# Performance work log

Hardware: AMD Instinct MI355X
Metric: run time of the kernel (lower is better)

## Reference

```python
import jax, jax.numpy as jnp
import numpy as np

TEXT_DIM = 768
IMAGE_DIM = 1024
HIDDEN = 2048
FF = 128
HEADS = 8
HEAD_DIM = HIDDEN // HEADS  # 256


def setup_inputs() -> dict:
    key = jax.random.key(0)
    ks = jax.random.split(key, 16)
    def lin(k, fan_in, fan_out):
        bound = 1.0 / np.sqrt(fan_in)
        kw, kb = jax.random.split(k)
        W = jax.random.uniform(kw, (fan_in, fan_out), jnp.float32, -bound, bound)
        b = jax.random.uniform(kb, (fan_out,), jnp.float32, -bound, bound)
        return W, b
    text = jax.random.normal(ks[0], (16, 512, TEXT_DIM), jnp.float32)
    image = jax.random.normal(ks[1], (16, 576, IMAGE_DIM), jnp.float32)
    wq, bq = lin(ks[2], TEXT_DIM, HIDDEN)
    wk, bk = lin(ks[3], IMAGE_DIM, HIDDEN)
    wv, bv = lin(ks[4], IMAGE_DIM, HIDDEN)
    wr, br = lin(ks[5], HIDDEN, TEXT_DIM)
    w1, b1 = lin(ks[6], TEXT_DIM, FF)
    w2, b2 = lin(ks[7], FF, TEXT_DIM)
    gamma = jnp.ones((TEXT_DIM,), jnp.float32)
    beta = jnp.zeros((TEXT_DIM,), jnp.float32)
    return {"text": text, "image": image,
            "wq": wq, "bq": bq, "wk": wk, "bk": bk, "wv": wv, "bv": bv,
            "wr": wr, "br": br, "w1": w1, "b1": b1, "w2": w2, "b2": b2,
            "gamma": gamma, "beta": beta}


def reference(text, image, wq, bq, wk, bk, wv, bv, wr, br, w1, b1, w2, b2, gamma, beta):
    # Dropout is identity (eval mode).
    bs, lt, _ = text.shape
    li = image.shape[1]
    Q = (text @ wq + bq).reshape(bs, lt, HEADS, HEAD_DIM)
    K = (image @ wk + bk).reshape(bs, li, HEADS, HEAD_DIM)
    V = (image @ wv + bv).reshape(bs, li, HEADS, HEAD_DIM)
    scale = jnp.sqrt(jnp.float32(HEAD_DIM))
    scores = jnp.einsum('bqhd,bkhd->bhqk', Q, K) / scale  # [B,H,Lt,Li]
    attn = jax.nn.softmax(scores, axis=-1)
    x = jnp.einsum('bhqk,bkhd->bqhd', attn, V).reshape(bs, lt, HIDDEN)
    out = x @ wr + br  # [B,Lt,text_dim]
    ff = jax.nn.relu(out @ w1 + b1) @ w2 + b2
    out = out + ff
    # LayerNorm over last dim (eps=1e-5, torch default)
    mu = jnp.mean(out, axis=-1, keepdims=True)
    var = jnp.mean(jnp.square(out - mu), axis=-1, keepdims=True)
    return (out - mu) / jnp.sqrt(var + 1e-5) * gamma + beta
```

## Files before the change

### kernel.cpp

```cpp
#include <hip/hip_runtime.h>
#include <stdint.h>
#include <stddef.h>

typedef __attribute__((ext_vector_type(8))) short bf16x8;
typedef __attribute__((ext_vector_type(4))) float f32x4;

typedef __attribute__((address_space(1))) unsigned int uint_g;
typedef __attribute__((address_space(3))) unsigned int uint_l;

#define DEV static __device__ __forceinline__

DEV unsigned short f2bf(float f) {
  unsigned int u = __float_as_uint(f);
  u += 0x7FFFu + ((u >> 16) & 1u);
  return (unsigned short)(u >> 16);
}

DEV void gl_lds16(const unsigned short* g, unsigned short* l) {
  __builtin_amdgcn_global_load_lds((const uint_g*)g, (uint_l*)l, 16, 0, 0);
}

__global__ __launch_bounds__(256) void k_f32_to_bf16(const float* __restrict__ in,
                                                     unsigned short* __restrict__ out, int n4) {
  int i = blockIdx.x * 256 + threadIdx.x;
  if (i >= n4) return;
  const float4 v = ((const float4*)in)[i];
  ushort4 o;
  o.x = f2bf(v.x); o.y = f2bf(v.y); o.z = f2bf(v.z); o.w = f2bf(v.w);
  ((ushort4*)out)[i] = o;
}

__global__ __launch_bounds__(256) void k_transpose_to_bf16(const float* __restrict__ in,
                                                           unsigned short* __restrict__ out,
                                                           int R, int C) {
  __shared__ unsigned short tile[32][33];
  const int c0 = blockIdx.x << 5, r0 = blockIdx.y << 5;
  const int tx = threadIdx.x & 31, ty = threadIdx.x >> 5;
  #pragma unroll
  for (int i = 0; i < 32; i += 8)
    tile[ty + i][tx] = f2bf(in[(size_t)(r0 + ty + i) * C + c0 + tx]);
  __syncthreads();
  #pragma unroll
  for (int i = 0; i < 32; i += 8)
    out[(size_t)(c0 + ty + i) * R + r0 + tx] = tile[tx][ty + i];
}

enum { EPI_BIAS = 0, EPI_VT = 3, EPI_DUAL = 4, EPI_RELU = 5, EPI_RES = 6, EPI_KV = 7 };

template <int EPI>
DEV void gemm8_body(unsigned short (&As)[2][16384], unsigned short (&Bs)[2][16384],
                    const unsigned short* __restrict__ A, const unsigned short* __restrict__ B,
                    int lda, int ldb, int kTiles,
                    void* C0, void* C1, const float* bias, const float* bias2,
                    int ldc, float scale, int bx, int by) {
  const int t = threadIdx.x;
  const int lane = t & 63, w = t >> 6;
  const int wm = w >> 2, wn = w & 3;
  const int frow = lane & 15, quad = lane >> 4;

  const unsigned short* Ab = A + (size_t)by * 256 * lda;
  const unsigned short* Bb = B + (size_t)bx * 256 * ldb;

  f32x4 acc[8][4] = {};

  auto stA = [&](int kt, int bi, int h) {
    #pragma unroll
    for (int it = 0; it < 2; ++it) {
      int e = (it << 9) + t;
      int row = (h << 7) + (e >> 3);
      int c16 = (e & 7) ^ (row & 7);
      gl_lds16(Ab + (size_t)row * lda + (kt << 6) + (c16 << 3),
               &As[bi][(row << 6) + ((e & 7) << 3)]);
    }
  };
  auto stB = [&](int kt, int bi, int h) {
    #pragma unroll
    for (int it = 0; it < 2; ++it) {
      int e = (it << 9) + t;
      int row = (h << 7) + (e >> 3);
      int c16 = (e & 7) ^ (row & 7);
      gl_lds16(Bb + (size_t)row * ldb + (kt << 6) + (c16 << 3),
               &Bs[bi][(row << 6) + ((e & 7) << 3)]);
    }
  };
  auto frag = [&](const unsigned short* buf, int row, int ksl) -> bf16x8 {
    int col = ((ksl << 5) + (quad << 3)) ^ ((row & 7) << 3);
    return *(const bf16x8*)&buf[(row << 6) + col];
  };

  stB(0, 0, 0); stB(0, 0, 1); stA(0, 0, 0); stA(0, 0, 1);
  if (kTiles > 1) {
    stB(1, 1, 0); stB(1, 1, 1); stA(1, 1, 0);
    asm volatile("s_waitcnt vmcnt(6)" ::: "memory");
  } else {
    asm volatile("s_waitcnt vmcnt(0)" ::: "memory");
  }
  asm volatile("s_barrier" ::: "memory");

  bf16x8 a[4][2], b0[2][2], b1[2][2];
  const int arow = wm << 7, brow = wn << 6;

  for (int kt = 0; kt < kTiles; ++kt) {
    const int pb = kt & 1, qb = pb ^ 1;
    const unsigned short* Ac = As[pb];
    const unsigned short* Bc = Bs[pb];

    #pragma unroll
    for (int m = 0; m < 4; ++m)
      #pragma unroll
      for (int k = 0; k < 2; ++k) a[m][k] = frag(Ac, arow + (m << 4) + frow, k);
    #pragma unroll
    for (int n = 0; n < 2; ++n)
      #pragma unroll
      for (int k = 0; k < 2; ++k) b0[n][k] = frag(Bc, brow + (n << 4) + frow, k);
    if (kt + 1 < kTiles) stA(kt + 1, qb, 1);
    asm volatile("s_barrier" ::: "memory");
    asm volatile("s_waitcnt lgkmcnt(0)" ::: "memory");
    __builtin_amdgcn_s_setprio(1);
    #pragma unroll
    for (int m = 0; m < 4; ++m)
      #pragma unroll
      for (int n = 0; n < 2; ++n)
        #pragma unroll
        for (int k = 0; k < 2; ++k)
          acc[m][n] = __builtin_amdgcn_mfma_f32_16x16x32_bf16(a[m][k], b0[n][k], acc[m][n], 0, 0, 0);
    __builtin_amdgcn_s_setprio(0);
    asm volatile("s_barrier" ::: "memory");

    #pragma unroll
    for (int n = 0; n < 2; ++n)
      #pragma unroll
      for (int k = 0; k < 2; ++k) b1[n][k] = frag(Bc, brow + 32 + (n << 4) + frow, k);
    if (kt + 2 < kTiles) stB(kt + 2, pb, 0);
    asm volatile("s_barrier" ::: "memory");
    asm volatile("s_waitcnt lgkmcnt(0)" ::: "memory");
    __builtin_amdgcn_s_setprio(1);
    #pragma unroll
    for (int m = 0; m < 4; ++m)
      #pragma unroll
      for (int n = 0; n < 2; ++n)
        #pragma unroll
        for (int k = 0; k < 2; ++k)
          acc[m][2 + n] = __builtin_amdgcn_mfma_f32_16x16x32_bf16(a[m][k], b1[n][k], acc[m][2 + n], 0, 0, 0);
    __builtin_amdgcn_s_setprio(0);
    asm volatile("s_barrier" ::: "memory");

    #pragma unroll
    for (int m = 0; m < 4; ++m)
      #pragma unroll
      for (int k = 0; k < 2; ++k) a[m][k] = frag(Ac, arow + 64 + (m << 4) + frow, k);
    if (kt + 2 < kTiles) stB(kt + 2, pb, 1);
    asm volatile("s_barrier" ::: "memory");
    asm volatile("s_waitcnt lgkmcnt(0)" ::: "memory");
    __builtin_amdgcn_s_setprio(1);
    #pragma unroll
    for (int m = 0; m < 4; ++m)
      #pragma unroll
      for (int n = 0; n < 2; ++n)
        #pragma unroll
        for (int k = 0; k < 2; ++k)
          acc[4 + m][n] = __builtin_amdgcn_mfma_f32_16x16x32_bf16(a[m][k], b0[n][k], acc[4 + m][n], 0, 0, 0);
    __builtin_amdgcn_s_setprio(0);
    asm volatile("s_barrier" ::: "memory");

    if (kt + 2 < kTiles) {
      stA(kt + 2, pb, 0);
      asm volatile("s_waitcnt vmcnt(6)" ::: "memory");
    } else if (kt + 1 < kTiles) {
      asm volatile("s_waitcnt vmcnt(0)" ::: "memory");
    }
    asm volatile("s_barrier" ::: "memory");
    __builtin_amdgcn_s_setprio(1);
    #pragma unroll
    for (int m = 0; m < 4; ++m)
      #pragma unroll
      for (int n = 0; n < 2; ++n)
        #pragma unroll
        for (int k = 0; k < 2; ++k)
          acc[4 + m][2 + n] = __builtin_amdgcn_mfma_f32_16x16x32_bf16(a[m][k], b1[n][k], acc[4 + m][2 + n], 0, 0, 0);
    __builtin_amdgcn_s_setprio(0);
    asm volatile("s_barrier" ::: "memory");
  }

  const int mb = by * 256 + wm * 128 + (quad << 2);
  const int nb = bx * 256 + wn * 64 + frow;
  #pragma unroll
  for (int mi = 0; mi < 8; ++mi) {
    const int m = mb + mi * 16;
    #pragma unroll
    for (int ni = 0; ni < 4; ++ni) {
      const int n = nb + ni * 16;
      f32x4 v = acc[mi][ni];
      if constexpr (EPI == EPI_BIAS) {
        unsigned short* O = (unsigned short*)C0;
        const float bv2 = bias[n];
        #pragma unroll
        for (int r = 0; r < 4; ++r) O[(size_t)(m + r) * ldc + n] = f2bf((v[r] + bv2) * scale);
      } else if constexpr (EPI == EPI_KV) {
        if (n < 2048) {
          unsigned short* O = (unsigned short*)C0;
          const float bv2 = bias[n];
          #pragma unroll
          for (int r = 0; r < 4; ++r) O[(size_t)(m + r) * ldc + n] = f2bf(v[r] + bv2);
        } else {
          const int n2 = n - 2048;
          const int b = m / 576, li = m - b * 576;
          const int h = n2 >> 8, d = n2 & 255;
          const float bv2 = bias2[n2];
          ushort4 o;
          o.x = f2bf(v[0] + bv2); o.y = f2bf(v[1] + bv2);
          o.z = f2bf(v[2] + bv2); o.w = f2bf(v[3] + bv2);
          *(ushort4*)((unsigned short*)C1 + ((size_t)((b * 8 + h) * 256 + d)) * 576 + li) = o;
        }
      }
    }
  }
}

__global__ __launch_bounds__(512, 2)
void k_qkv(const unsigned short* __restrict__ Tbf, const unsigned short* __restrict__ wqT,
           unsigned short* Qb, const float* bq, float qscale,
           const unsigned short* __restrict__ Ibf, const unsigned short* __restrict__ wkT,
           unsigned short* Kb, unsigned short* Vt, const float* bk, const float* bv) {
  __shared__ unsigned short As[2][16384];
  __shared__ unsigned short Bs[2][16384];
  const int id = blockIdx.x;
  if (id < 576) {
    gemm8_body<EPI_KV>(As, Bs, Ibf, wkT, 1024, 1024, 16,
                       Kb, Vt, bk, bv, 2048, 1.0f, id & 15, id >> 4);
  } else {
    const int q = id - 576;
    gemm8_body<EPI_BIAS>(As, Bs, Tbf, wqT, 768, 768, 12,
                         Qb, nullptr, bq, nullptr, 2048, qscale, q & 7, q >> 3);
  }
}

template <int BM, int BN, int EPI>
__global__ __launch_bounds__(256)
void k_gemm(const unsigned short* __restrict__ A, const unsigned short* __restrict__ B,
            int lda, int ldb, int kSteps,
            void* C0, void* C1, const float* bias, const float* resid, int ldc, float scale) {
  constexpr int TM = BM / 32;
  constexpr int TN = BN / 32;
  __shared__ unsigned short At[2][BM * 32];
  __shared__ unsigned short Bt[2][BN * 32];

  const int t = threadIdx.x;
  const int lane = t & 63, wave = t >> 6;
  const int wm = wave >> 1, wn = wave & 1;

  const unsigned short* Ab = A + (size_t)blockIdx.y * BM * lda;
  const unsigned short* Bb = B + (size_t)blockIdx.x * BN * ldb;

  const int frow = lane & 15, fk = (lane >> 4) << 3;

  f32x4 acc[TM][TN] = {};

  auto stage = [&](int ks, int bi) {
    const int k0 = ks << 5;
    #pragma unroll
    for (int r = 0; r < BM / 64; ++r) {
      int off16 = (r << 8) + t;
      int row = off16 >> 2, kk = (off16 & 3) << 3;
      gl_lds16(Ab + (size_t)row * lda + k0 + kk, &At[bi][(row << 5) + kk]);
    }
    #pragma unroll
    for (int r = 0; r < BN / 64; ++r) {
      int off16 = (r << 8) + t;
      int row = off16 >> 2, kk = (off16 & 3) << 3;
      gl_lds16(Bb + (size_t)row * ldb + k0 + kk, &Bt[bi][(row << 5) + kk]);
    }
  };

  stage(0, 0);

  for (int ks = 0; ks < kSteps; ++ks) {
    const int buf = ks & 1;
    __syncthreads();
    if (ks + 1 < kSteps) stage(ks + 1, buf ^ 1);

    bf16x8 af[TM], bv[TN];
    #pragma unroll
    for (int mi = 0; mi < TM; ++mi)
      af[mi] = *(const bf16x8*)&At[buf][((wm * (BM / 2) + mi * 16 + frow) << 5) + fk];
    #pragma unroll
    for (int ni = 0; ni < TN; ++ni)
      bv[ni] = *(const bf16x8*)&Bt[buf][((wn * (BN / 2) + ni * 16 + frow) << 5) + fk];
    #pragma unroll
    for (int mi = 0; mi < TM; ++mi)
      #pragma unroll
      for (int ni = 0; ni < TN; ++ni)
        acc[mi][ni] = __builtin_amdgcn_mfma_f32_16x16x32_bf16(af[mi], bv[ni], acc[mi][ni], 0, 0, 0);
  }

  const int mb = blockIdx.y * BM + wm * (BM / 2) + ((lane >> 4) << 2);
  const int nb = blockIdx.x * BN + wn * (BN / 2) + (lane & 15);

  #pragma unroll
  for (int mi = 0; mi < TM; ++mi) {
    const int m = mb + mi * 16;
    #pragma unroll
    for (int ni = 0; ni < TN; ++ni) {
      const int n = nb + ni * 16;
      f32x4 v = acc[mi][ni];
      if constexpr (EPI == EPI_BIAS) {
        unsigned short* O = (unsigned short*)C0;
        const float bv2 = bias[n];
        #pragma unroll
        for (int r = 0; r < 4; ++r) O[(size_t)(m + r) * ldc + n] = f2bf((v[r] + bv2) * scale);
      } else if constexpr (EPI == EPI_DUAL) {
        float* Of = (float*)C0;
        unsigned short* Ob = (unsigned short*)C1;
        const float bv2 = bias[n];
        #pragma unroll
        for (int r = 0; r < 4; ++r) {
          const float x = v[r] + bv2;
          const size_t idx = (size_t)(m + r) * ldc + n;
          Of[idx] = x; Ob[idx] = f2bf(x);
        }
      } else if constexpr (EPI == EPI_RELU) {
        unsigned short* O = (unsigned short*)C0;
        const float bv2 = bias[n];
        #pragma unroll
        for (int r = 0; r < 4; ++r) {
          const float x = v[r] + bv2;
          O[(size_t)(m + r) * ldc + n] = f2bf(x > 0.f ? x : 0.f);
        }
      } else if constexpr (EPI == EPI_RES) {
        float* Of = (float*)C0;
        const float bv2 = bias[n];
        #pragma unroll
        for (int r = 0; r < 4; ++r) {
          const size_t idx = (size_t)(m + r) * ldc + n;
          Of[idx] = v[r] + bv2 + resid[idx];
        }
      }
    }
  }
}

__global__ __launch_bounds__(512, 2)
void k_flash(const unsigned short* __restrict__ Q, const unsigned short* __restrict__ K,
             const unsigned short* __restrict__ Vt, unsigned short* __restrict__ X) {
  __shared__ unsigned short Ks[2][8 * 32 * 32];
  __shared__ unsigned short Vs[2][256 * 32];
  __shared__ unsigned short Ps[256 * 40];
  __shared__ unsigned short Ones[512];

  const int t = threadIdx.x, lane = t & 63, w = t >> 6;
  const int frow = lane & 15, quad = lane >> 4, fk = quad << 3;

  const int id = blockIdx.x;
  const int qb = (id >> 3) & 1;
  const int bh = (id & 7) | ((id >> 4) << 3);
  const int b = bh >> 3, h = bh & 7;
  const int q0 = qb << 8;

  const unsigned short* Kg = K + ((size_t)b * 576) * 2048 + h * 256;
  const unsigned short* Vg = Vt + (size_t)bh * 147456;

  Ones[t] = (t < 32) ? (unsigned short)0x3F80 : (unsigned short)0;

  bf16x8 Qf[2][8];
  #pragma unroll
  for (int half = 0; half < 2; ++half) {
    const unsigned short* Qg =
        Q + ((size_t)(b * 512 + q0 + w * 32 + half * 16 + frow)) * 2048 + h * 256;
    #pragma unroll
    for (int kd = 0; kd < 8; ++kd)
      Qf[half][kd] = *(const bf16x8*)(Qg + kd * 32 + fk);
  }

  f32x4 acc_o[2][17] = {};

  auto stage = [&](int s, int bi) {
    const int li0 = s << 5;
    unsigned short* Kb = &Ks[bi][0];
    unsigned short* Vb = &Vs[bi][0];
    #pragma unroll
    for (int it = 0; it < 2; ++it) {
      int e = (it << 9) + t;
      int row = e >> 2, c = (e & 3) << 3;
      int kd = row >> 5, li = row & 31;
      gl_lds16(Kg + (size_t)(li0 + li) * 2048 + kd * 32 + c, &Kb[(row << 5) + c]);
    }
    #pragma unroll
    for (int it = 0; it < 2; ++it) {
      int e = (it << 9) + t;
      int d = e >> 2, c = (e & 3) << 3;
      gl_lds16(Vg + (size_t)d * 576 + li0 + c, &Vb[(d << 5) + c]);
    }
  };

  stage(0, 0);

  const int prow = (w << 5) + (quad << 2);

  for (int s = 0; s < 18; ++s) {
    const int buf = s & 1;
    __syncthreads();
    if (s + 1 < 18) stage(s + 1, buf ^ 1);

    f32x4 acc_s[2][2] = {};
    #pragma unroll
    for (int kd = 0; kd < 8; ++kd) {
      #pragma unroll
      for (int ni = 0; ni < 2; ++ni) {
        const bf16x8 bv = *(const bf16x8*)&Ks[buf][((kd * 32 + ni * 16 + frow) << 5) + fk];
        acc_s[0][ni] = __builtin_amdgcn_mfma_f32_16x16x32_bf16(Qf[0][kd], bv, acc_s[0][ni], 0, 0, 0);
        acc_s[1][ni] = __builtin_amdgcn_mfma_f32_16x16x32_bf16(Qf[1][kd], bv, acc_s[1][ni], 0, 0, 0);
      }
    }

    #pragma unroll
    for (int half = 0; half < 2; ++half)
      #pragma unroll
      for (int ni = 0; ni < 2; ++ni)
        #pragma unroll
        for (int r = 0; r < 4; ++r)
          Ps[(prow + half * 16 + r) * 40 + ni * 16 + frow] =
              f2bf(__builtin_amdgcn_exp2f(acc_s[half][ni][r]));

    bf16x8 paf[2];
    paf[0] = *(const bf16x8*)&Ps[((w << 5) + frow) * 40 + fk];
    paf[1] = *(const bf16x8*)&Ps[((w << 5) + 16 + frow) * 40 + fk];
    #pragma unroll
    for (int ni = 0; ni < 16; ++ni) {
      const bf16x8 bv = *(const bf16x8*)&Vs[buf][((ni * 16 + frow) << 5) + fk];
      acc_o[0][ni] = __builtin_amdgcn_mfma_f32_16x16x32_bf16(paf[0], bv, acc_o[0][ni], 0, 0, 0);
      acc_o[1][ni] = __builtin_amdgcn_mfma_f32_16x16x32_bf16(paf[1], bv, acc_o[1][ni], 0, 0, 0);
    }
    {
      const bf16x8 bv = *(const bf16x8*)&Ones[(frow << 5) + fk];
      acc_o[0][16] = __builtin_amdgcn_mfma_f32_16x16x32_bf16(paf[0], bv, acc_o[0][16], 0, 0, 0);
      acc_o[1][16] = __builtin_amdgcn_mfma_f32_16x16x32_bf16(paf[1], bv, acc_o[1][16], 0, 0, 0);
    }
  }

  #pragma unroll
  for (int half = 0; half < 2; ++half) {
    float linv[4];
    #pragma unroll
    for (int r = 0; r < 4; ++r)
      linv[r] = 1.0f / __shfl(acc_o[half][16][r], lane & 48);
    unsigned short* Xo = X + ((size_t)(b * 512 + q0 + w * 32 + half * 16 + (quad << 2))) * 2048 +
                         h * 256 + frow;
    #pragma unroll
    for (int ni = 0; ni < 16; ++ni)
      #pragma unroll
      for (int r = 0; r < 4; ++r)
        Xo[(size_t)r * 2048 + ni * 16] = f2bf(acc_o[half][ni][r] * linv[r]);
  }
}

__global__ __launch_bounds__(256) void k_layernorm768(float* O, const float* __restrict__ gamma,
                                                      const float* __restrict__ beta) {
  const int row = blockIdx.x;
  float* p = O + (size_t)row * 768;
  const int t = threadIdx.x;
  const int lane = t & 63, wave = t >> 6;
  const float x0 = p[t], x1 = p[t + 256], x2 = p[t + 512];
  float s = x0 + x1 + x2;
  float q = x0 * x0 + x1 * x1 + x2 * x2;
  #pragma unroll
  for (int i = 32; i >= 1; i >>= 1) { s += __shfl_xor(s, i); q += __shfl_xor(q, i); }
  __shared__ float rs[4], rq[4];
  if (lane == 0) { rs[wave] = s; rq[wave] = q; }
  __syncthreads();
  s = rs[0] + rs[1] + rs[2] + rs[3];
  q = rq[0] + rq[1] + rq[2] + rq[3];
  const float mu = s * (1.0f / 768.0f);
  const float var = q * (1.0f / 768.0f) - mu * mu;
  const float inv = rsqrtf(var + 1e-5f);
  p[t]       = (x0 - mu) * inv * gamma[t]       + beta[t];
  p[t + 256] = (x1 - mu) * inv * gamma[t + 256] + beta[t + 256];
  p[t + 512] = (x2 - mu) * inv * gamma[t + 512] + beta[t + 512];
}

extern "C" void kernel_launch(void* const* d_in, const int* in_sizes, int n_in,
                              void* d_out, int out_size, void* d_ws, size_t ws_size,
                              hipStream_t stream) {
  const float* text  = (const float*)d_in[0];
  const float* image = (const float*)d_in[1];
  const float* wq = (const float*)d_in[2];  const float* bq = (const float*)d_in[3];
  const float* wk = (const float*)d_in[4];  const float* bk = (const float*)d_in[5];
  const float* wv = (const float*)d_in[6];  const float* bv = (const float*)d_in[7];
  const float* wr = (const float*)d_in[8];  const float* br = (const float*)d_in[9];
  const float* w1 = (const float*)d_in[10]; const float* b1 = (const float*)d_in[11];
  const float* w2 = (const float*)d_in[12]; const float* b2 = (const float*)d_in[13];
  const float* gamma = (const float*)d_in[14]; const float* beta = (const float*)d_in[15];

  uint8_t* ws = (uint8_t*)d_ws;
  constexpr size_t o_Tbf = 0;
  constexpr size_t o_Ibf = 12582912;
  constexpr size_t o_X   = 0;
  constexpr size_t o_Q   = 33554432;
  constexpr size_t o_Kb  = o_Q   + 33554432;
  constexpr size_t o_Vt  = o_Kb  + 37748736;
  constexpr size_t o_wqT = o_Vt  + 37748736;
  constexpr size_t o_wkT = o_wqT + 3145728;
  constexpr size_t o_wvT = o_wkT + 4194304;
  constexpr size_t o_wrT = o_wvT + 4194304;
  constexpr size_t o_w1T = o_wrT + 3145728;
  constexpr size_t o_w2T = o_w1T + 196608;
  constexpr size_t o_OutB= o_w2T + 196608;
  constexpr size_t o_H   = o_OutB+ 12582912;

  unsigned short* Tbf  = (unsigned short*)(ws + o_Tbf);
  unsigned short* Ibf  = (unsigned short*)(ws + o_Ibf);
  unsigned short* Xb   = (unsigned short*)(ws + o_X);
  unsigned short* Qb   = (unsigned short*)(ws + o_Q);
  unsigned short* Kb   = (unsigned short*)(ws + o_Kb);
  unsigned short* Vt   = (unsigned short*)(ws + o_Vt);
  unsigned short* wqT  = (unsigned short*)(ws + o_wqT);
  unsigned short* wkT  = (unsigned short*)(ws + o_wkT);
  unsigned short* wvT  = (unsigned short*)(ws + o_wvT);
  unsigned short* wrT  = (unsigned short*)(ws + o_wrT);
  unsigned short* w1T  = (unsigned short*)(ws + o_w1T);
  unsigned short* w2T  = (unsigned short*)(ws + o_w2T);
  unsigned short* OutB = (unsigned short*)(ws + o_OutB);
  unsigned short* Hb   = (unsigned short*)(ws + o_H);
  float* OutF = (float*)d_out;

  const dim3 blk(256);

  k_f32_to_bf16<<<dim3(6144), blk, 0, stream>>>(text,  Tbf, 1572864);
  k_f32_to_bf16<<<dim3(9216), blk, 0, stream>>>(image, Ibf, 2359296);
  k_transpose_to_bf16<<<dim3(64, 24), blk, 0, stream>>>(wq, wqT, 768, 2048);
  k_transpose_to_bf16<<<dim3(64, 32), blk, 0, stream>>>(wk, wkT, 1024, 2048);
  k_transpose_to_bf16<<<dim3(64, 32), blk, 0, stream>>>(wv, wvT, 1024, 2048);
  k_transpose_to_bf16<<<dim3(24, 64), blk, 0, stream>>>(wr, wrT, 2048, 768);
  k_transpose_to_bf16<<<dim3(4, 24),  blk, 0, stream>>>(w1, w1T, 768, 128);
  k_transpose_to_bf16<<<dim3(24, 4),  blk, 0, stream>>>(w2, w2T, 128, 768);

  k_qkv<<<dim3(832), dim3(512), 0, stream>>>(
      Tbf, wqT, Qb, bq, 0.0625f * 1.44269504f,
      Ibf, wkT, Kb, Vt, bk, bv);

  k_flash<<<dim3(256), dim3(512), 0, stream>>>(Qb, Kb, Vt, Xb);

  k_gemm<128, 128, EPI_DUAL><<<dim3(6, 64), blk, 0, stream>>>(
      Xb, wrT, 2048, 2048, 64, OutF, OutB, br, nullptr, 768, 1.0f);

  k_gemm<64, 64, EPI_RELU><<<dim3(2, 128), blk, 0, stream>>>(
      OutB, w1T, 768, 768, 24, Hb, nullptr, b1, nullptr, 128, 1.0f);

  k_gemm<128, 128, EPI_RES><<<dim3(6, 64), blk, 0, stream>>>(
      Hb, w2T, 128, 128, 4, OutF, nullptr, b2, (const float*)d_out, 768, 1.0f);

  k_layernorm768<<<dim3(8192), blk, 0, stream>>>(OutF, gamma, beta);

  (void)in_sizes; (void)n_in; (void)out_size; (void)ws_size;
}
```

Before: 455.0 us.

## Fuse FF2 GEMM with residual and LayerNorm, merge conversion and transpose launches

Replaces the separate FF2 GEMM with residual epilogue and the standalone LayerNorm kernel with one kernel. Each block computes 32 full rows of 768 outputs by MFMA, adds bias and residual, reduces the row statistics through shuffles and shared memory, and writes the normalized result. This avoids a full fp32 round trip of the output through memory and one launch. The two input conversions are merged into one launch and the six weight transposes into another, cutting launch overhead. The fused kernel launches only 256 blocks and reads its operands straight from global memory without LDS staging, which may leave the GPU underoccupied.

```diff
diff --git a/kernel.cpp b/kernel.cpp
--- a/kernel.cpp
+++ b/kernel.cpp
@@ -20,21 +20,36 @@
   __builtin_amdgcn_global_load_lds((const uint_g*)g, (uint_l*)l, 16, 0, 0);
 }
 
-__global__ __launch_bounds__(256) void k_f32_to_bf16(const float* __restrict__ in,
-                                                     unsigned short* __restrict__ out, int n4) {
-  int i = blockIdx.x * 256 + threadIdx.x;
-  if (i >= n4) return;
+__global__ __launch_bounds__(256) void k_convert2(const float* __restrict__ a,
+                                                  unsigned short* __restrict__ oa,
+                                                  const float* __restrict__ b,
+                                                  unsigned short* __restrict__ ob) {
+  const int id = blockIdx.x;
+  const float* in;  unsigned short* out;  int i;
+  if (id < 6144) { in = a; out = oa; i = id * 256 + threadIdx.x; }
+  else           { in = b; out = ob; i = (id - 6144) * 256 + threadIdx.x; }
   const float4 v = ((const float4*)in)[i];
   ushort4 o;
   o.x = f2bf(v.x); o.y = f2bf(v.y); o.z = f2bf(v.z); o.w = f2bf(v.w);
   ((ushort4*)out)[i] = o;
 }
 
-__global__ __launch_bounds__(256) void k_transpose_to_bf16(const float* __restrict__ in,
-                                                           unsigned short* __restrict__ out,
-                                                           int R, int C) {
+__global__ __launch_bounds__(256) void k_transpose_all(
+    const float* __restrict__ wq, const float* __restrict__ wk,
+    const float* __restrict__ wv, const float* __restrict__ wr,
+    const float* __restrict__ w1, const float* __restrict__ w2,
+    unsigned short* wqT, unsigned short* wkT, unsigned short* wvT,
+    unsigned short* wrT, unsigned short* w1T, unsigned short* w2T) {
   __shared__ unsigned short tile[32][33];
-  const int c0 = blockIdx.x << 5, r0 = blockIdx.y << 5;
+  int id = blockIdx.x;
+  const float* in; unsigned short* out; int R, C, bx, by;
+  if (id < 1536)      {            in = wq; out = wqT; R = 768;  C = 2048; bx = id & 63; by = id >> 6; }
+  else if (id < 3584) { id -= 1536; in = wk; out = wkT; R = 1024; C = 2048; bx = id & 63; by = id >> 6; }
+  else if (id < 5632) { id -= 3584; in = wv; out = wvT; R = 1024; C = 2048; bx = id & 63; by = id >> 6; }
+  else if (id < 7168) { id -= 5632; in = wr; out = wrT; R = 2048; C = 768;  bx = id % 24; by = id / 24; }
+  else if (id < 7264) { id -= 7168; in = w1; out = w1T; R = 768;  C = 128;  bx = id & 3;  by = id >> 2; }
+  else                { id -= 7264; in = w2; out = w2T; R = 128;  C = 768;  bx = id % 24; by = id / 24; }
+  const int c0 = bx << 5, r0 = by << 5;
   const int tx = threadIdx.x & 31, ty = threadIdx.x >> 5;
   #pragma unroll
   for (int i = 0; i < 32; i += 8)
@@ -45,7 +60,7 @@
     out[(size_t)(c0 + ty + i) * R + r0 + tx] = tile[tx][ty + i];
 }
 
-enum { EPI_BIAS = 0, EPI_VT = 3, EPI_DUAL = 4, EPI_RELU = 5, EPI_RES = 6, EPI_KV = 7 };
+enum { EPI_BIAS = 0, EPI_VT = 3, EPI_DUAL = 4, EPI_RELU = 5, EPI_KV = 7 };
 
 template <int EPI>
 DEV void gemm8_body(unsigned short (&As)[2][16384], unsigned short (&Bs)[2][16384],
@@ -326,14 +341,6 @@
           const float x = v[r] + bv2;
           O[(size_t)(m + r) * ldc + n] = f2bf(x > 0.f ? x : 0.f);
         }
-      } else if constexpr (EPI == EPI_RES) {
-        float* Of = (float*)C0;
-        const float bv2 = bias[n];
-        #pragma unroll
-        for (int r = 0; r < 4; ++r) {
-          const size_t idx = (size_t)(m + r) * ldc + n;
-          Of[idx] = v[r] + bv2 + resid[idx];
-        }
       }
     }
   }
@@ -453,28 +460,81 @@
   }
 }
 
-__global__ __launch_bounds__(256) void k_layernorm768(float* O, const float* __restrict__ gamma,
-                                                      const float* __restrict__ beta) {
-  const int row = blockIdx.x;
-  float* p = O + (size_t)row * 768;
-  const int t = threadIdx.x;
-  const int lane = t & 63, wave = t >> 6;
-  const float x0 = p[t], x1 = p[t + 256], x2 = p[t + 512];
-  float s = x0 + x1 + x2;
-  float q = x0 * x0 + x1 * x1 + x2 * x2;
-  #pragma unroll
-  for (int i = 32; i >= 1; i >>= 1) { s += __shfl_xor(s, i); q += __shfl_xor(q, i); }
-  __shared__ float rs[4], rq[4];
-  if (lane == 0) { rs[wave] = s; rq[wave] = q; }
+__global__ __launch_bounds__(256)
+void k_ff2_ln(const unsigned short* __restrict__ Hb, const unsigned short* __restrict__ w2T,
+              const float* __restrict__ b2, float* __restrict__ Out,
+              const float* __restrict__ gamma, const float* __restrict__ beta) {
+  const int t = threadIdx.x, lane = t & 63, w = t >> 6;
+  const int frow = lane & 15, quad = lane >> 4, fk = quad << 3;
+  const int m0 = blockIdx.x << 5;
+
+  f32x4 acc[2][12] = {};
+  #pragma unroll
+  for (int ks = 0; ks < 4; ++ks) {
+    bf16x8 a[2];
+    #pragma unroll
+    for (int mi = 0; mi < 2; ++mi)
+      a[mi] = *(const bf16x8*)(Hb + (size_t)(m0 + mi * 16 + frow) * 128 + ks * 32 + fk);
+    #pragma unroll
+    for (int ni = 0; ni < 12; ++ni) {
+      const bf16x8 b = *(const bf16x8*)(w2T + (size_t)(w * 192 + ni * 16 + frow) * 128 + ks * 32 + fk);
+      acc[0][ni] = __builtin_amdgcn_mfma_f32_16x16x32_bf16(a[0], b, acc[0][ni], 0, 0, 0);
+      acc[1][ni] = __builtin_amdgcn_mfma_f32_16x16x32_bf16(a[1], b, acc[1][ni], 0, 0, 0);
+    }
+  }
+
+  float s8[2][4] = {}, q8[2][4] = {};
+  #pragma unroll
+  for (int mi = 0; mi < 2; ++mi)
+    #pragma unroll
+    for (int ni = 0; ni < 12; ++ni) {
+      const int n = w * 192 + ni * 16 + frow;
+      const float bv = b2[n];
+      #pragma unroll
+      for (int r = 0; r < 4; ++r) {
+        const int row = m0 + mi * 16 + (quad << 2) + r;
+        const float x = acc[mi][ni][r] + bv + Out[(size_t)row * 768 + n];
+        acc[mi][ni][r] = x;
+        s8[mi][r] += x; q8[mi][r] += x * x;
+      }
+    }
+  #pragma unroll
+  for (int msk = 1; msk <= 8; msk <<= 1)
+    #pragma unroll
+    for (int mi = 0; mi < 2; ++mi)
+      #pragma unroll
+      for (int r = 0; r < 4; ++r) {
+        s8[mi][r] += __shfl_xor(s8[mi][r], msk);
+        q8[mi][r] += __shfl_xor(q8[mi][r], msk);
+      }
+  __shared__ float redS[4][32], redQ[4][32];
+  if (frow == 0) {
+    #pragma unroll
+    for (int mi = 0; mi < 2; ++mi)
+      #pragma unroll
+      for (int r = 0; r < 4; ++r) {
+        const int r32 = mi * 16 + (quad << 2) + r;
+        redS[w][r32] = s8[mi][r]; redQ[w][r32] = q8[mi][r];
+      }
+  }
   __syncthreads();
-  s = rs[0] + rs[1] + rs[2] + rs[3];
-  q = rq[0] + rq[1] + rq[2] + rq[3];
-  const float mu = s * (1.0f / 768.0f);
-  const float var = q * (1.0f / 768.0f) - mu * mu;
-  const float inv = rsqrtf(var + 1e-5f);
-  p[t]       = (x0 - mu) * inv * gamma[t]       + beta[t];
-  p[t + 256] = (x1 - mu) * inv * gamma[t + 256] + beta[t + 256];
-  p[t + 512] = (x2 - mu) * inv * gamma[t + 512] + beta[t + 512];
+  #pragma unroll
+  for (int mi = 0; mi < 2; ++mi)
+    #pragma unroll
+    for (int r = 0; r < 4; ++r) {
+      const int r32 = mi * 16 + (quad << 2) + r;
+      const float S = redS[0][r32] + redS[1][r32] + redS[2][r32] + redS[3][r32];
+      const float Qq = redQ[0][r32] + redQ[1][r32] + redQ[2][r32] + redQ[3][r32];
+      const float mu = S * (1.0f / 768.0f);
+      const float var = Qq * (1.0f / 768.0f) - mu * mu;
+      const float inv = rsqrtf(var + 1e-5f);
+      const size_t rowoff = (size_t)(m0 + r32) * 768;
+      #pragma unroll
+      for (int ni = 0; ni < 12; ++ni) {
+        const int n = w * 192 + ni * 16 + frow;
+        Out[rowoff + n] = (acc[mi][ni][r] - mu) * inv * gamma[n] + beta[n];
+      }
+    }
 }
 
 extern "C" void kernel_launch(void* const* d_in, const int* in_sizes, int n_in,
@@ -524,14 +584,9 @@
 
   const dim3 blk(256);
 
-  k_f32_to_bf16<<<dim3(6144), blk, 0, stream>>>(text,  Tbf, 1572864);
-  k_f32_to_bf16<<<dim3(9216), blk, 0, stream>>>(image, Ibf, 2359296);
-  k_transpose_to_bf16<<<dim3(64, 24), blk, 0, stream>>>(wq, wqT, 768, 2048);
-  k_transpose_to_bf16<<<dim3(64, 32), blk, 0, stream>>>(wk, wkT, 1024, 2048);
-  k_transpose_to_bf16<<<dim3(64, 32), blk, 0, stream>>>(wv, wvT, 1024, 2048);
-  k_transpose_to_bf16<<<dim3(24, 64), blk, 0, stream>>>(wr, wrT, 2048, 768);
-  k_transpose_to_bf16<<<dim3(4, 24),  blk, 0, stream>>>(w1, w1T, 768, 128);
-  k_transpose_to_bf16<<<dim3(24, 4),  blk, 0, stream>>>(w2, w2T, 128, 768);
+  k_convert2<<<dim3(15360), blk, 0, stream>>>(text, Tbf, image, Ibf);
+  k_transpose_all<<<dim3(7360), blk, 0, stream>>>(wq, wk, wv, wr, w1, w2,
+                                                  wqT, wkT, wvT, wrT, w1T, w2T);
 
   k_qkv<<<dim3(832), dim3(512), 0, stream>>>(
       Tbf, wqT, Qb, bq, 0.0625f * 1.44269504f,
@@ -545,10 +600,7 @@
   k_gemm<64, 64, EPI_RELU><<<dim3(2, 128), blk, 0, stream>>>(
       OutB, w1T, 768, 768, 24, Hb, nullptr, b1, nullptr, 128, 1.0f);
 
-  k_gemm<128, 128, EPI_RES><<<dim3(6, 64), blk, 0, stream>>>(
-      Hb, w2T, 128, 128, 4, OutF, nullptr, b2, (const float*)d_out, 768, 1.0f);
-
-  k_layernorm768<<<dim3(8192), blk, 0, stream>>>(OutF, gamma, beta);
+  k_ff2_ln<<<dim3(256), blk, 0, stream>>>(Hb, w2T, b2, OutF, gamma, beta);
 
   (void)in_sizes; (void)n_in; (void)out_size; (void)ws_size;
 }
```

Result: faster. 425.6 us (-6.5%).
